# Kernel tuning notes

Measured on AMD Instinct MI355X. Metric: run time of the kernel, lower is better.

Reference implementation:

```python
import jax, jax.numpy as jnp
import numpy as np

N_TOKENS = 8192
HIDDEN = 4096
N_EXPERTS = 64
TOP_K = 8


def setup_inputs() -> dict:
    key = jax.random.key(0)
    k1, k2 = jax.random.split(key)
    h = jax.random.normal(k1, (N_TOKENS, HIDDEN), dtype=jnp.float32)
    weight = jax.random.normal(k2, (N_EXPERTS, HIDDEN), dtype=jnp.float32) * (1.0 / np.sqrt(HIDDEN))
    return {"h": h, "weight": weight}


def reference(h, weight):
    # logits = h @ W^T in fp32  -> [n_tokens, n_experts]
    logits = jnp.einsum("th,eh->te", h.astype(jnp.float32), weight.astype(jnp.float32))
    scores = jax.nn.softmax(logits, axis=-1)
    topk_weight, topk_idx = jax.lax.top_k(scores, TOP_K)  # [n_tokens, k]
    return topk_weight, topk_idx
```

## Files before the change

### kernel.cpp

```cpp
#include <hip/hip_runtime.h>
#include <math.h>
#include <stdint.h>

#define NTOK 8192
#define HID  4096
#define NEXP 64
#define TOPK 8

typedef float    f32x4 __attribute__((ext_vector_type(4)));
typedef _Float16 f16x8 __attribute__((ext_vector_type(8)));


__device__ __forceinline__ void cvt_hilo(f32x4 a, f32x4 b, f16x8& hi, f16x8& lo)
{
    float x[8] = {a.x, a.y, a.z, a.w, b.x, b.y, b.z, b.w};
#pragma unroll
    for (int j = 0; j < 8; ++j) {
        const _Float16 h = (_Float16)x[j];
        hi[j] = h;
        lo[j] = (_Float16)(x[j] - (float)h);
    }
}

__device__ __forceinline__ void gll16(const void* g, void* l) {
    __builtin_amdgcn_global_load_lds(
        (const __attribute__((address_space(1))) uint32_t*)g,
        (__attribute__((address_space(3))) uint32_t*)l, 16, 0, 0);
}

__global__ __launch_bounds__(256)
void k0_pack(const float* __restrict__ W, f16x8* __restrict__ wq)
{
    const int gidx = blockIdx.x * 256 + threadIdx.x;
    const int s = gidx >> 8;
    const int E = (gidx >> 6) & 3;
    const int l = gidx & 63;
    const int e = E * 16 + (l & 15);
    const int k = s * 32 + ((l >> 4) << 3);

    const float* src = W + (size_t)e * HID + k;
    const f32x4 w0 = *(const f32x4*)src;
    const f32x4 w1 = *(const f32x4*)(src + 4);
    f16x8 hi, lo;
    cvt_hilo(w0 * 2048.0f, w1 * 2048.0f, hi, lo);

    wq[s * 512 + E * 128 + l]      = hi;
    wq[s * 512 + E * 128 + 64 + l] = lo;
}

#define ALD(S, GS) do { const float* _p = ha + (GS) * 32;                     \
    A##S##0 = *(const f32x4*)_p; A##S##1 = *(const f32x4*)(_p + 4); } while (0)

#define BLD(S, STEP) do { const _Float16* _q = &BL[(STEP) * 4096];            \
    Bh##S##0 = *(const f16x8*)&_q[           l * 8];                          \
    Bl##S##0 = *(const f16x8*)&_q[ 512 +     l * 8];                          \
    Bh##S##1 = *(const f16x8*)&_q[1024 +     l * 8];                          \
    Bl##S##1 = *(const f16x8*)&_q[1536 +     l * 8];                          \
    Bh##S##2 = *(const f16x8*)&_q[2048 +     l * 8];                          \
    Bl##S##2 = *(const f16x8*)&_q[2560 +     l * 8];                          \
    Bh##S##3 = *(const f16x8*)&_q[3072 +     l * 8];                          \
    Bl##S##3 = *(const f16x8*)&_q[3584 +     l * 8]; } while (0)

#define CSTEP(AS, BS) do { f16x8 _ah, _al; cvt_hilo(A##AS##0, A##AS##1, _ah, _al); \
    acH0 = __builtin_amdgcn_mfma_f32_16x16x32_f16(_ah, Bh##BS##0, acH0, 0, 0, 0); \
    acH1 = __builtin_amdgcn_mfma_f32_16x16x32_f16(_ah, Bh##BS##1, acH1, 0, 0, 0); \
    acH2 = __builtin_amdgcn_mfma_f32_16x16x32_f16(_ah, Bh##BS##2, acH2, 0, 0, 0); \
    acH3 = __builtin_amdgcn_mfma_f32_16x16x32_f16(_ah, Bh##BS##3, acH3, 0, 0, 0); \
    acC0 = __builtin_amdgcn_mfma_f32_16x16x32_f16(_ah, Bl##BS##0, acC0, 0, 0, 0); \
    acC1 = __builtin_amdgcn_mfma_f32_16x16x32_f16(_ah, Bl##BS##1, acC1, 0, 0, 0); \
    acC2 = __builtin_amdgcn_mfma_f32_16x16x32_f16(_ah, Bl##BS##2, acC2, 0, 0, 0); \
    acC3 = __builtin_amdgcn_mfma_f32_16x16x32_f16(_ah, Bl##BS##3, acC3, 0, 0, 0); \
    acC0 = __builtin_amdgcn_mfma_f32_16x16x32_f16(_al, Bh##BS##0, acC0, 0, 0, 0); \
    acC1 = __builtin_amdgcn_mfma_f32_16x16x32_f16(_al, Bh##BS##1, acC1, 0, 0, 0); \
    acC2 = __builtin_amdgcn_mfma_f32_16x16x32_f16(_al, Bh##BS##2, acC2, 0, 0, 0); \
    acC3 = __builtin_amdgcn_mfma_f32_16x16x32_f16(_al, Bh##BS##3, acC3, 0, 0, 0); \
} while (0)

#define Q(S, AS, BS) do { CSTEP(AS, BS);                                      \
    if ((S) + 4 < 16) ALD(AS, (S) + 4);                                       \
    if ((S) + 2 < 16) BLD(BS, (S) + 2); } while (0)

__global__ __launch_bounds__(512, 1)
void k1_logits(const float* __restrict__ Hm, const f16x8* __restrict__ wq,
               float* __restrict__ lgp)
{
    __shared__ _Float16 BL[65536];

    const int tid  = threadIdx.x;
    const int w    = tid >> 6;
    const int l    = tid & 63;
    const int tg   = blockIdx.x >> 3;
    const int ks   = blockIdx.x & 7;
    const int tok0 = tg * 128 + w * 16;
    const int kb   = ks * 512;

    const char* wsrc = (const char*)wq + (size_t)ks * 131072;
#pragma unroll
    for (int t = 0; t < 16; ++t)
        gll16(wsrc + t * 8192 + tid * 16, (char*)BL + t * 8192 + tid * 16);
    __syncthreads();

    const float* ha = Hm + (size_t)(tok0 + (l & 15)) * HID + kb + ((l >> 4) << 3);

    f32x4 acH0 = (f32x4)(0.f), acH1 = (f32x4)(0.f), acH2 = (f32x4)(0.f), acH3 = (f32x4)(0.f);
    f32x4 acC0 = (f32x4)(0.f), acC1 = (f32x4)(0.f), acC2 = (f32x4)(0.f), acC3 = (f32x4)(0.f);

    f32x4 Aa0, Aa1, Ab0, Ab1, Ac0, Ac1, Ad0, Ad1;
    f16x8 Bhx0, Bhx1, Bhx2, Bhx3, Blx0, Blx1, Blx2, Blx3;
    f16x8 Bhy0, Bhy1, Bhy2, Bhy3, Bly0, Bly1, Bly2, Bly3;

    ALD(a, 0); ALD(b, 1); ALD(c, 2); ALD(d, 3);
    BLD(x, 0); BLD(y, 1);

    Q( 0, a, x); Q( 1, b, y); Q( 2, c, x); Q( 3, d, y);
    Q( 4, a, x); Q( 5, b, y); Q( 6, c, x); Q( 7, d, y);
    Q( 8, a, x); Q( 9, b, y); Q(10, c, x); Q(11, d, y);
    Q(12, a, x); Q(13, b, y); Q(14, c, x); Q(15, d, y);

    float* o = lgp + ((size_t)ks * NTOK + tok0) * 64;
    {
        const f32x4 v0 = acH0 + acC0, v1 = acH1 + acC1,
                    v2 = acH2 + acC2, v3 = acH3 + acC3;
#pragma unroll
        for (int r = 0; r < 4; ++r) {
            const int trow = ((l >> 4) << 2) + r;
            o[trow * 64 +  0 + (l & 15)] = v0[r];
            o[trow * 64 + 16 + (l & 15)] = v1[r];
            o[trow * 64 + 32 + (l & 15)] = v2[r];
            o[trow * 64 + 48 + (l & 15)] = v3[r];
        }
    }
}

__global__ __launch_bounds__(256)
void k2_finish(const float* __restrict__ lgp, float* __restrict__ out)
{
    __shared__ __align__(16) float sc[4][64];
    const int tid  = threadIdx.x;
    const int wave = tid >> 6;
    const int lane = tid & 63;
    float* outw = out;
    float* outi = out + (size_t)NTOK * TOPK;

    const int tok = blockIdx.x * 4 + wave;
    const float* p = lgp + (size_t)tok * 64 + lane;
    const size_t SL = (size_t)NTOK * 64;
    const float lgv = (((p[0] + p[SL]) + (p[2*SL] + p[3*SL]))
                     + ((p[4*SL] + p[5*SL]) + (p[6*SL] + p[7*SL])))
                     * (1.0f / 2048.0f);

    float mx = lgv;
#pragma unroll
    for (int off = 32; off; off >>= 1) mx = fmaxf(mx, __shfl_xor(mx, off));
    const float pv = expf(lgv - mx);
    float ss = pv;
#pragma unroll
    for (int off = 32; off; off >>= 1) ss += __shfl_xor(ss, off);
    ss = __shfl(ss, 0);
    const float sval = pv / ss;

    sc[wave][lane] = sval;
    __syncthreads();

    int rank = 0;
#pragma unroll
    for (int j4 = 0; j4 < 16; ++j4) {
        const f32x4 v = *(const f32x4*)&sc[wave][j4 * 4];
#pragma unroll
        for (int u = 0; u < 4; ++u) {
            const int j = j4 * 4 + u;
            rank += (v[u] > sval || (v[u] == sval && j < lane)) ? 1 : 0;
        }
    }
    if (rank < TOPK) {
        outw[(size_t)tok * TOPK + rank] = sval;
        outi[(size_t)tok * TOPK + rank] = (float)lane;
    }
}

extern "C" void kernel_launch(void* const* d_in, const int* in_sizes, int n_in,
                              void* d_out, int out_size, void* d_ws, size_t ws_size,
                              hipStream_t stream) {
    (void)in_sizes; (void)n_in; (void)out_size; (void)ws_size;
    const float* h = (const float*)d_in[0];
    const float* w = (const float*)d_in[1];
    float* out = (float*)d_out;

    f16x8* wq  = (f16x8*)d_ws;
    float* lgp = (float*)((char*)d_ws + (1 << 20));

    k0_pack<<<128, 256, 0, stream>>>(w, wq);
    k1_logits<<<512, 512, 0, stream>>>(h, wq, lgp);
    k2_finish<<<NTOK / 4, 256, 0, stream>>>(lgp, out);
}
```

Before: 43.44 us.

## Stream H and W tiles through swizzled LDS ring with async loads

The logits kernel now stages both the activation and packed weight tiles through a 4-slot LDS ring using global_load_lds, prefetching two k-steps ahead and synchronising with an explicit waitcnt and barrier per step. Previously the whole weight slice was loaded into LDS up front and H was read directly into registers. The block decomposition also changes: 64 tokens by 1024 k per block with a 4-way K split instead of 8, waves split over tokens and expert halves, and launch bounds allow 2 blocks per CU. The finish kernel now sums 4 partials instead of 8. The risks are a barrier every k-step and the XOR swizzle bookkeeping.

Result: faster. 39.62 us (median of 2 runs) (-8.8%).

```diff
diff --git a/kernel.cpp b/kernel.cpp
--- a/kernel.cpp
+++ b/kernel.cpp
@@ -28,6 +28,9 @@
         (__attribute__((address_space(3))) uint32_t*)l, 16, 0, 0);
 }
 
+#define MFMA16(AH, BH, AC) \
+    AC = __builtin_amdgcn_mfma_f32_16x16x32_f16(AH, BH, AC, 0, 0, 0)
+
 __global__ __launch_bounds__(256)
 void k0_pack(const float* __restrict__ W, f16x8* __restrict__ wq)
 {
@@ -48,87 +51,82 @@
     wq[s * 512 + E * 128 + 64 + l] = lo;
 }
 
-#define ALD(S, GS) do { const float* _p = ha + (GS) * 32;                     \
-    A##S##0 = *(const f32x4*)_p; A##S##1 = *(const f32x4*)(_p + 4); } while (0)
-
-#define BLD(S, STEP) do { const _Float16* _q = &BL[(STEP) * 4096];            \
-    Bh##S##0 = *(const f16x8*)&_q[           l * 8];                          \
-    Bl##S##0 = *(const f16x8*)&_q[ 512 +     l * 8];                          \
-    Bh##S##1 = *(const f16x8*)&_q[1024 +     l * 8];                          \
-    Bl##S##1 = *(const f16x8*)&_q[1536 +     l * 8];                          \
-    Bh##S##2 = *(const f16x8*)&_q[2048 +     l * 8];                          \
-    Bl##S##2 = *(const f16x8*)&_q[2560 +     l * 8];                          \
-    Bh##S##3 = *(const f16x8*)&_q[3072 +     l * 8];                          \
-    Bl##S##3 = *(const f16x8*)&_q[3584 +     l * 8]; } while (0)
-
-#define CSTEP(AS, BS) do { f16x8 _ah, _al; cvt_hilo(A##AS##0, A##AS##1, _ah, _al); \
-    acH0 = __builtin_amdgcn_mfma_f32_16x16x32_f16(_ah, Bh##BS##0, acH0, 0, 0, 0); \
-    acH1 = __builtin_amdgcn_mfma_f32_16x16x32_f16(_ah, Bh##BS##1, acH1, 0, 0, 0); \
-    acH2 = __builtin_amdgcn_mfma_f32_16x16x32_f16(_ah, Bh##BS##2, acH2, 0, 0, 0); \
-    acH3 = __builtin_amdgcn_mfma_f32_16x16x32_f16(_ah, Bh##BS##3, acH3, 0, 0, 0); \
-    acC0 = __builtin_amdgcn_mfma_f32_16x16x32_f16(_ah, Bl##BS##0, acC0, 0, 0, 0); \
-    acC1 = __builtin_amdgcn_mfma_f32_16x16x32_f16(_ah, Bl##BS##1, acC1, 0, 0, 0); \
-    acC2 = __builtin_amdgcn_mfma_f32_16x16x32_f16(_ah, Bl##BS##2, acC2, 0, 0, 0); \
-    acC3 = __builtin_amdgcn_mfma_f32_16x16x32_f16(_ah, Bl##BS##3, acC3, 0, 0, 0); \
-    acC0 = __builtin_amdgcn_mfma_f32_16x16x32_f16(_al, Bh##BS##0, acC0, 0, 0, 0); \
-    acC1 = __builtin_amdgcn_mfma_f32_16x16x32_f16(_al, Bh##BS##1, acC1, 0, 0, 0); \
-    acC2 = __builtin_amdgcn_mfma_f32_16x16x32_f16(_al, Bh##BS##2, acC2, 0, 0, 0); \
-    acC3 = __builtin_amdgcn_mfma_f32_16x16x32_f16(_al, Bh##BS##3, acC3, 0, 0, 0); \
+#define STAGE2(S) do {                                                        \
+    gll16(hap + (size_t)(S) * 128,  &LDSB[((S) % 4) * 8192 + tid * 16]);      \
+    gll16(bap + (size_t)(S) * 8192, &LDSB[32768 + ((S) % 4) * 8192 + tid * 16]); \
 } while (0)
 
-#define Q(S, AS, BS) do { CSTEP(AS, BS);                                      \
-    if ((S) + 4 < 16) ALD(AS, (S) + 4);                                       \
-    if ((S) + 2 < 16) BLD(BS, (S) + 2); } while (0)
+#define KSTEP(S, VN) do {                                                     \
+    if ((S) + 2 < 32) STAGE2((S) + 2);                                        \
+    asm volatile("s_waitcnt vmcnt(" #VN ")" ::: "memory");                    \
+    __builtin_amdgcn_sched_barrier(0);                                        \
+    __builtin_amdgcn_s_barrier();                                             \
+    __builtin_amdgcn_sched_barrier(0);                                        \
+    const char* _A = &LDSB[((S) % 4) * 8192];                                 \
+    const char* _B = &LDSB[32768 + ((S) % 4) * 8192];                         \
+    const f32x4 a0 = *(const f32x4*)&_A[ga0 * 16];                            \
+    const f32x4 a1 = *(const f32x4*)&_A[ga1 * 16];                            \
+    const f16x8 bh0 = *(const f16x8*)&_B[(E0 * 128 + l) * 16];                \
+    const f16x8 bl0 = *(const f16x8*)&_B[(E0 * 128 + 64 + l) * 16];           \
+    const f16x8 bh1 = *(const f16x8*)&_B[(E1 * 128 + l) * 16];                \
+    const f16x8 bl1 = *(const f16x8*)&_B[(E1 * 128 + 64 + l) * 16];           \
+    f16x8 _ah, _al; cvt_hilo(a0, a1, _ah, _al);                               \
+    MFMA16(_ah, bh0, acH0); MFMA16(_ah, bh1, acH1);                           \
+    MFMA16(_ah, bl0, acC0); MFMA16(_ah, bl1, acC1);                           \
+    MFMA16(_al, bh0, acC0); MFMA16(_al, bh1, acC1);                           \
+} while (0)
 
-__global__ __launch_bounds__(512, 1)
-void k1_logits(const float* __restrict__ Hm, const f16x8* __restrict__ wq,
+__global__ __launch_bounds__(512, 2)
+void k1_logits(const float* __restrict__ Hm, const char* __restrict__ wqc,
                float* __restrict__ lgp)
 {
-    __shared__ _Float16 BL[65536];
+    __shared__ char LDSB[65536];
 
     const int tid  = threadIdx.x;
-    const int w    = tid >> 6;
+    const int wave = tid >> 6;
     const int l    = tid & 63;
-    const int tg   = blockIdx.x >> 3;
-    const int ks   = blockIdx.x & 7;
-    const int tok0 = tg * 128 + w * 16;
-    const int kb   = ks * 512;
+    const int kg   = l >> 4;
+    const int tg   = wave >> 1;
+    const int eg   = wave & 1;
+    const int E0   = eg * 2;
+    const int E1   = eg * 2 + 1;
+    const int tokg = blockIdx.x >> 2;
+    const int ksb  = blockIdx.x & 3;
+    const int tok0 = tokg * 64;
+    const int kb   = ksb * 1024;
 
-    const char* wsrc = (const char*)wq + (size_t)ks * 131072;
+    const int tloc = tg * 16 + (l & 15);
+    const int ga0  = tloc * 8 + ((kg * 2)     ^ (l & 7));
+    const int ga1  = tloc * 8 + ((kg * 2 + 1) ^ (l & 7));
+
+    const int st = tid >> 3;
+    const int so = tid & 7;
+    const char* hap = (const char*)(Hm + (size_t)(tok0 + st) * HID + kb)
+                    + ((so ^ (st & 7)) * 16);
+    const char* bap = wqc + (size_t)ksb * 262144 + tid * 16;
+
+    f32x4 acH0 = (f32x4)(0.f), acH1 = (f32x4)(0.f);
+    f32x4 acC0 = (f32x4)(0.f), acC1 = (f32x4)(0.f);
+
+    STAGE2(0); STAGE2(1);
+
+    KSTEP( 0, 4); KSTEP( 1, 4); KSTEP( 2, 4); KSTEP( 3, 4);
+    KSTEP( 4, 4); KSTEP( 5, 4); KSTEP( 6, 4); KSTEP( 7, 4);
+    KSTEP( 8, 4); KSTEP( 9, 4); KSTEP(10, 4); KSTEP(11, 4);
+    KSTEP(12, 4); KSTEP(13, 4); KSTEP(14, 4); KSTEP(15, 4);
+    KSTEP(16, 4); KSTEP(17, 4); KSTEP(18, 4); KSTEP(19, 4);
+    KSTEP(20, 4); KSTEP(21, 4); KSTEP(22, 4); KSTEP(23, 4);
+    KSTEP(24, 4); KSTEP(25, 4); KSTEP(26, 4); KSTEP(27, 4);
+    KSTEP(28, 4); KSTEP(29, 4); KSTEP(30, 2); KSTEP(31, 0);
+
+    const f32x4 v0 = acH0 + acC0;
+    const f32x4 v1 = acH1 + acC1;
+    float* o = lgp + ((size_t)ksb * NTOK + tok0 + tg * 16) * 64 + eg * 32;
 #pragma unroll
-    for (int t = 0; t < 16; ++t)
-        gll16(wsrc + t * 8192 + tid * 16, (char*)BL + t * 8192 + tid * 16);
-    __syncthreads();
-
-    const float* ha = Hm + (size_t)(tok0 + (l & 15)) * HID + kb + ((l >> 4) << 3);
-
-    f32x4 acH0 = (f32x4)(0.f), acH1 = (f32x4)(0.f), acH2 = (f32x4)(0.f), acH3 = (f32x4)(0.f);
-    f32x4 acC0 = (f32x4)(0.f), acC1 = (f32x4)(0.f), acC2 = (f32x4)(0.f), acC3 = (f32x4)(0.f);
-
-    f32x4 Aa0, Aa1, Ab0, Ab1, Ac0, Ac1, Ad0, Ad1;
-    f16x8 Bhx0, Bhx1, Bhx2, Bhx3, Blx0, Blx1, Blx2, Blx3;
-    f16x8 Bhy0, Bhy1, Bhy2, Bhy3, Bly0, Bly1, Bly2, Bly3;
-
-    ALD(a, 0); ALD(b, 1); ALD(c, 2); ALD(d, 3);
-    BLD(x, 0); BLD(y, 1);
-
-    Q( 0, a, x); Q( 1, b, y); Q( 2, c, x); Q( 3, d, y);
-    Q( 4, a, x); Q( 5, b, y); Q( 6, c, x); Q( 7, d, y);
-    Q( 8, a, x); Q( 9, b, y); Q(10, c, x); Q(11, d, y);
-    Q(12, a, x); Q(13, b, y); Q(14, c, x); Q(15, d, y);
-
-    float* o = lgp + ((size_t)ks * NTOK + tok0) * 64;
-    {
-        const f32x4 v0 = acH0 + acC0, v1 = acH1 + acC1,
-                    v2 = acH2 + acC2, v3 = acH3 + acC3;
-#pragma unroll
-        for (int r = 0; r < 4; ++r) {
-            const int trow = ((l >> 4) << 2) + r;
-            o[trow * 64 +  0 + (l & 15)] = v0[r];
-            o[trow * 64 + 16 + (l & 15)] = v1[r];
-            o[trow * 64 + 32 + (l & 15)] = v2[r];
-            o[trow * 64 + 48 + (l & 15)] = v3[r];
-        }
+    for (int r = 0; r < 4; ++r) {
+        const int row = (kg << 2) + r;
+        o[row * 64 +      (l & 15)] = v0[r];
+        o[row * 64 + 16 + (l & 15)] = v1[r];
     }
 }
 
@@ -145,9 +143,7 @@
     const int tok = blockIdx.x * 4 + wave;
     const float* p = lgp + (size_t)tok * 64 + lane;
     const size_t SL = (size_t)NTOK * 64;
-    const float lgv = (((p[0] + p[SL]) + (p[2*SL] + p[3*SL]))
-                     + ((p[4*SL] + p[5*SL]) + (p[6*SL] + p[7*SL])))
-                     * (1.0f / 2048.0f);
+    const float lgv = ((p[0] + p[SL]) + (p[2 * SL] + p[3 * SL])) * (1.0f / 2048.0f);
 
     float mx = lgv;
 #pragma unroll
@@ -190,6 +186,6 @@
     float* lgp = (float*)((char*)d_ws + (1 << 20));
 
     k0_pack<<<128, 256, 0, stream>>>(w, wq);
-    k1_logits<<<512, 512, 0, stream>>>(h, wq, lgp);
+    k1_logits<<<512, 512, 0, stream>>>(h, (const char*)wq, lgp);
     k2_finish<<<NTOK / 4, 256, 0, stream>>>(lgp, out);
 }
```
